# Optimization experiments

Hardware: AMD Instinct MI355X
Metric: run time of the kernel (lower is better)

Reference implementation:

```python
import jax, jax.numpy as jnp
import numpy as np

N, D, H, ED, E = 50000, 128, 4, 16, 800000
C = D // H  # 32 per-head channels


def setup_inputs() -> dict:
    key = jax.random.key(0)
    ks = jax.random.split(key, 12)
    w = lambda k, shape: jax.random.normal(k, shape, jnp.float32) * 0.05
    z = lambda: jnp.zeros((D,), jnp.float32)
    return dict(
        x=jax.random.normal(ks[0], (N, D), jnp.float32),
        edge_index=jax.random.randint(ks[1], (2, E), 0, N),
        edge_attr=jax.random.normal(ks[2], (E, ED), jnp.float32),
        Wq=w(ks[3], (D, D)), bq=z(),
        Wk=w(ks[4], (D, D)), bk=z(),
        Wv=w(ks[5], (D, D)), bv=z(),
        We=w(ks[6], (ED, D)),              # lin_edge, bias=False in PyG
        Ws=w(ks[7], (D, D)), bs=z(),       # TransformerConv root/skip lin
        Wsp=w(ks[8], (D, D)), bsp=z(),     # skip_proj
        Wg=w(ks[9], (2 * D, D)), bg=z(),   # gate linear
        g1=jnp.ones((D,), jnp.float32), b1=z(),
        g2=jnp.ones((D,), jnp.float32), b2=z(),
    )


def _ln(x, g, b):
    mu = x.mean(-1, keepdims=True)
    var = ((x - mu) ** 2).mean(-1, keepdims=True)
    return (x - mu) * jax.lax.rsqrt(var + 1e-5) * g + b


def reference(x, edge_index, edge_attr, Wq, bq, Wk, bk, Wv, bv, We, Ws, bs,
              Wsp, bsp, Wg, bg, g1, b1, g2, b2):
    src, dst = edge_index[0], edge_index[1]  # PyG: row=source j, col=target i
    q = (x @ Wq + bq).reshape(N, H, C)
    k = (x @ Wk + bk).reshape(N, H, C)
    v = (x @ Wv + bv).reshape(N, H, C)
    e = (edge_attr @ We).reshape(E, H, C)

    k_j = k[src] + e                                   # [E,H,C]
    alpha = (q[dst] * k_j).sum(-1) / np.sqrt(C)        # [E,H]
    # segment softmax over incoming edges of each target node
    m = jax.ops.segment_max(alpha, dst, num_segments=N)
    ea = jnp.exp(alpha - m[dst])
    denom = jax.ops.segment_sum(ea, dst, num_segments=N)
    a = ea / (denom[dst] + 1e-16)                      # [E,H]

    msg = (v[src] + e) * a[..., None]                  # [E,H,C]
    agg = jax.ops.segment_sum(msg, dst, num_segments=N).reshape(N, D)
    h = agg + x @ Ws + bs                              # root_weight skip

    h = jax.nn.gelu(_ln(h, g1, b1), approximate=False)  # norm1 + GELU (dropout=eval no-op)
    skip = x @ Wsp + bsp
    gate = jax.nn.sigmoid(jnp.concatenate([h, x], axis=1) @ Wg + bg)
    h = gate * h + (1.0 - gate) * skip
    return _ln(h, g2, b2)
```

## Files before the change

kernel.cpp:

```cpp
#include <hip/hip_runtime.h>
#include <hip/hip_bf16.h>

typedef short short8 __attribute__((ext_vector_type(8)));
typedef float f32x4 __attribute__((ext_vector_type(4)));

__device__ inline unsigned short f2bf(float x) {
  union { float f; unsigned u; } un; un.f = x;
  unsigned r = un.u + 0x7FFFu + ((un.u >> 16) & 1u);
  return (unsigned short)(r >> 16);
}
__device__ inline float bf2f(unsigned short u) {
  union { unsigned u; float f; } un; un.u = ((unsigned)u) << 16; return un.f;
}

__global__ void prep_weights(const float* __restrict__ Wq, const float* __restrict__ bq,
                             const float* __restrict__ Wk, const float* __restrict__ bk,
                             const float* __restrict__ Wv, const float* __restrict__ bv,
                             const float* __restrict__ Ws, const float* __restrict__ bs,
                             const float* __restrict__ Wsp, const float* __restrict__ bsp,
                             const float* __restrict__ Wg, const float* __restrict__ bg,
                             unsigned short* __restrict__ WcatT, unsigned short* __restrict__ WgTopT,
                             float* __restrict__ bcat) {
  int tid = blockIdx.x * 256 + threadIdx.x;
  if (tid >= 768 * 128) return;
  int n = tid >> 7, k = tid & 127;
  int s = n >> 7, c = n & 127;
  float val;
  if (s == 0) val = Wq[k * 128 + c];
  else if (s == 1) val = Wk[k * 128 + c];
  else if (s == 2) val = Wv[k * 128 + c];
  else if (s == 3) val = Ws[k * 128 + c];
  else if (s == 4) val = Wsp[k * 128 + c];
  else val = Wg[(128 + k) * 128 + c];
  WcatT[tid] = f2bf(val);
  if (n < 128) WgTopT[n * 128 + k] = f2bf(Wg[k * 128 + n]);
  if (k == 0) {
    float bv2;
    if (s == 0) bv2 = bq[c]; else if (s == 1) bv2 = bk[c]; else if (s == 2) bv2 = bv[c];
    else if (s == 3) bv2 = bs[c]; else if (s == 4) bv2 = bsp[c]; else bv2 = bg[c];
    bcat[n] = bv2;
  }
}

__global__ void prep_wefrag(const float* __restrict__ We, unsigned short* __restrict__ wf) {
  int id = blockIdx.x * 256 + threadIdx.x;
  if (id >= 4096) return;
  int j = id & 7, lane = (id >> 3) & 63, b = id >> 9;
  int t = (lane >> 4) * 8 + j;
  float v = (t < 16) ? We[t * 128 + b * 16 + (lane & 15)] : 0.0f;
  wf[id] = f2bf(v);
}

__global__ void convert_bf16(const float* __restrict__ x, unsigned short* __restrict__ xb, int n4) {
  int i = blockIdx.x * 256 + threadIdx.x;
  if (i < n4) {
    float4 v = ((const float4*)x)[i];
    ushort4 o;
    o.x = f2bf(v.x); o.y = f2bf(v.y); o.z = f2bf(v.z); o.w = f2bf(v.w);
    ((ushort4*)xb)[i] = o;
  }
}

__global__ void count_deg(const int* __restrict__ dst, int* __restrict__ deg, int E) {
  int i = blockIdx.x * 256 + threadIdx.x;
  if (i < E) atomicAdd(&deg[dst[i]], 1);
}

__global__ __launch_bounds__(256) void scan_bsum(const int* __restrict__ deg, int* __restrict__ bsum, int n) {
  __shared__ int red[256];
  int b = blockIdx.x, t = threadIdx.x;
  int base = b * 1024 + t * 4;
  int s = 0;
#pragma unroll
  for (int j = 0; j < 4; ++j) { int i = base + j; if (i < n) s += deg[i]; }
  red[t] = s; __syncthreads();
  for (int o = 128; o; o >>= 1) { if (t < o) red[t] += red[t + o]; __syncthreads(); }
  if (t == 0) bsum[b] = red[0];
}

__global__ void scan_top(int* __restrict__ bsum, int G) {
  int lane = threadIdx.x;
  int v = (lane < G) ? bsum[lane] : 0;
  int orig = v;
#pragma unroll
  for (int d = 1; d < 64; d <<= 1) { int u = __shfl_up(v, d); if (lane >= d) v += u; }
  if (lane < G) bsum[lane] = v - orig;
}

__global__ __launch_bounds__(256) void scan_write(const int* __restrict__ deg, const int* __restrict__ bsum,
                                                  int* __restrict__ off, int* __restrict__ cursor, int n) {
  __shared__ int red[256];
  int b = blockIdx.x, t = threadIdx.x;
  int base = b * 1024 + t * 4;
  int d0 = 0, d1 = 0, d2 = 0, d3 = 0;
  if (base + 3 < n) {
    int4 d4 = *(const int4*)(deg + base);
    d0 = d4.x; d1 = d4.y; d2 = d4.z; d3 = d4.w;
  } else {
    if (base + 0 < n) d0 = deg[base + 0];
    if (base + 1 < n) d1 = deg[base + 1];
    if (base + 2 < n) d2 = deg[base + 2];
    if (base + 3 < n) d3 = deg[base + 3];
  }
  int tsum = d0 + d1 + d2 + d3;
  red[t] = tsum; __syncthreads();
  for (int o = 1; o < 256; o <<= 1) {
    int val = (t >= o) ? red[t - o] : 0;
    __syncthreads();
    red[t] += val;
    __syncthreads();
  }
  int run = bsum[b] + red[t] - tsum;
  if (base + 0 < n) { off[base + 0] = run; cursor[base + 0] = run; run += d0; }
  if (base + 1 < n) { off[base + 1] = run; cursor[base + 1] = run; run += d1; }
  if (base + 2 < n) { off[base + 2] = run; cursor[base + 2] = run; run += d2; }
  if (base + 3 < n) { off[base + 3] = run; cursor[base + 3] = run; run += d3; }
  if (b == gridDim.x - 1 && t == 255) off[n] = run;
}

__global__ void scatter_kernel(const int* __restrict__ ei, int* __restrict__ cursor,
                               int2* __restrict__ slotsrc, int E) {
  int i = blockIdx.x * 256 + threadIdx.x;
  if (i < E) {
    int s = ei[i];
    int d = ei[E + i];
    int p = atomicAdd(&cursor[d], 1);
    slotsrc[p] = make_int2(i, s);
  }
}

__global__ __launch_bounds__(256) void gemm_fused(const unsigned short* __restrict__ A,
                                                  const unsigned short* __restrict__ BT,
                                                  const float* __restrict__ bias,
                                                  float* __restrict__ Y, int M) {
  __shared__ char As[32768];
  __shared__ char Bs[32768];
  int m0 = blockIdx.x * 128;
  int t = threadIdx.x;
  {
    int row = t >> 1;
    int hb = (t & 1) * 128;
    const char* srow = (const char*)(A + (size_t)(m0 + row) * 128);
    bool ok = (m0 + row) < M;
    char* lrow = As + row * 256;
    int sw = (row & 7) << 4;
#pragma unroll
    for (int j = 0; j < 8; ++j) {
      int b = hb + j * 16;
      uint4 val;
      if (ok) val = *(const uint4*)(srow + b);
      else { val.x = 0; val.y = 0; val.z = 0; val.w = 0; }
      *(uint4*)(lrow + (b ^ sw)) = val;
    }
  }
  int w = t >> 6, lane = t & 63;
  int lm = lane & 15, hi = lane >> 4;
  for (int nb = 0; nb < 6; ++nb) {
    __syncthreads();
    {
      int row = t >> 1;
      int hb = (t & 1) * 128;
      const char* srow = (const char*)(BT + (size_t)(nb * 128 + row) * 128);
      char* lrow = Bs + row * 256;
      int sw = (row & 7) << 4;
#pragma unroll
      for (int j = 0; j < 8; ++j) {
        int b = hb + j * 16;
        uint4 val = *(const uint4*)(srow + b);
        *(uint4*)(lrow + (b ^ sw)) = val;
      }
    }
    __syncthreads();
    f32x4 acc[2][8] = {};
#pragma unroll
    for (int kb = 0; kb < 4; ++kb) {
      int colb = kb * 64 + hi * 16;
      short8 a[2];
#pragma unroll
      for (int rf = 0; rf < 2; ++rf) {
        int row = w * 32 + rf * 16 + lm;
        a[rf] = *(const short8*)(As + row * 256 + (colb ^ ((row & 7) << 4)));
      }
#pragma unroll
      for (int cf = 0; cf < 8; ++cf) {
        int row = cf * 16 + lm;
        short8 bfr = *(const short8*)(Bs + row * 256 + (colb ^ ((row & 7) << 4)));
        acc[0][cf] = __builtin_amdgcn_mfma_f32_16x16x32_bf16(a[0], bfr, acc[0][cf], 0, 0, 0);
        acc[1][cf] = __builtin_amdgcn_mfma_f32_16x16x32_bf16(a[1], bfr, acc[1][cf], 0, 0, 0);
      }
    }
    bool to16 = (nb == 1 || nb == 2);
#pragma unroll
    for (int rf = 0; rf < 2; ++rf) {
#pragma unroll
      for (int cf = 0; cf < 8; ++cf) {
        int col = nb * 128 + cf * 16 + lm;
        float bv = bias[col];
#pragma unroll
        for (int j = 0; j < 4; ++j) {
          int row = m0 + w * 32 + rf * 16 + hi * 4 + j;
          if (row < M) {
            float val = acc[rf][cf][j] + bv;
            if (to16) {
              unsigned short* kvrow = (unsigned short*)((char*)Y + (size_t)row * 3072 + 512);
              kvrow[col - 128] = f2bf(val);
            } else {
              Y[(size_t)row * 768 + col] = val;
            }
          }
        }
      }
    }
  }
}

__global__ __launch_bounds__(256) void gemm_single(const unsigned short* __restrict__ A,
                                                   const unsigned short* __restrict__ BT,
                                                   float* __restrict__ C, int M) {
  __shared__ char As[32768];
  __shared__ char Bs[32768];
  int m0 = blockIdx.x * 128;
  int t = threadIdx.x;
  {
    int row = t >> 1;
    int hb = (t & 1) * 128;
    const char* srow = (const char*)(A + (size_t)(m0 + row) * 128);
    bool ok = (m0 + row) < M;
    char* lrow = As + row * 256;
    int sw = (row & 7) << 4;
#pragma unroll
    for (int j = 0; j < 8; ++j) {
      int b = hb + j * 16;
      uint4 val;
      if (ok) val = *(const uint4*)(srow + b);
      else { val.x = 0; val.y = 0; val.z = 0; val.w = 0; }
      *(uint4*)(lrow + (b ^ sw)) = val;
    }
  }
  {
    int row = t >> 1;
    int hb = (t & 1) * 128;
    const char* srow = (const char*)(BT + (size_t)row * 128);
    char* lrow = Bs + row * 256;
    int sw = (row & 7) << 4;
#pragma unroll
    for (int j = 0; j < 8; ++j) {
      int b = hb + j * 16;
      uint4 val = *(const uint4*)(srow + b);
      *(uint4*)(lrow + (b ^ sw)) = val;
    }
  }
  __syncthreads();
  int w = t >> 6, lane = t & 63;
  int lm = lane & 15, hi = lane >> 4;
  f32x4 acc[2][8] = {};
#pragma unroll
  for (int kb = 0; kb < 4; ++kb) {
    int colb = kb * 64 + hi * 16;
    short8 a[2];
#pragma unroll
    for (int rf = 0; rf < 2; ++rf) {
      int row = w * 32 + rf * 16 + lm;
      a[rf] = *(const short8*)(As + row * 256 + (colb ^ ((row & 7) << 4)));
    }
#pragma unroll
    for (int cf = 0; cf < 8; ++cf) {
      int row = cf * 16 + lm;
      short8 bfr = *(const short8*)(Bs + row * 256 + (colb ^ ((row & 7) << 4)));
      acc[0][cf] = __builtin_amdgcn_mfma_f32_16x16x32_bf16(a[0], bfr, acc[0][cf], 0, 0, 0);
      acc[1][cf] = __builtin_amdgcn_mfma_f32_16x16x32_bf16(a[1], bfr, acc[1][cf], 0, 0, 0);
    }
  }
#pragma unroll
  for (int rf = 0; rf < 2; ++rf) {
#pragma unroll
    for (int cf = 0; cf < 8; ++cf) {
      int col = cf * 16 + lm;
#pragma unroll
      for (int j = 0; j < 4; ++j) {
        int row = m0 + w * 32 + rf * 16 + hi * 4 + j;
        if (row < M) C[(size_t)row * 128 + col] = acc[rf][cf][j];
      }
    }
  }
}

__global__ __launch_bounds__(256) void edge_flash(const int2* __restrict__ slotsrc,
                                                  const int* __restrict__ off,
                                                  const unsigned short* __restrict__ attrb,
                                                  const unsigned short* __restrict__ wefrag,
                                                  const float* __restrict__ Y,
                                                  float* __restrict__ agg, int Nn) {
  int wv = threadIdx.x >> 6, lane = threadIdx.x & 63;
  int node = blockIdx.x * 4 + wv;
  if (node >= Nn) return;
  int esl = lane & 15, hi = lane >> 4;

  short8 weF[8];
#pragma unroll
  for (int b = 0; b < 8; ++b)
    weF[b] = *(const short8*)(wefrag + ((b * 64 + lane) << 3));

  float qv[8][4];
  const float* qrow = Y + (size_t)node * 768;
#pragma unroll
  for (int b = 0; b < 8; ++b) {
    float4 tq = *(const float4*)(qrow + 16 * b + 4 * hi);
    qv[b][0] = tq.x * 0.25505654f;
    qv[b][1] = tq.y * 0.25505654f;
    qv[b][2] = tq.z * 0.25505654f;
    qv[b][3] = tq.w * 0.25505654f;
  }

  float m[4], den[4], agr[8][4];
#pragma unroll
  for (int h = 0; h < 4; ++h) { m[h] = -INFINITY; den[h] = 0.0f; }
#pragma unroll
  for (int b = 0; b < 8; ++b)
#pragma unroll
    for (int r = 0; r < 4; ++r) agr[b][r] = 0.0f;

  int beg = off[node], end = off[node + 1];
  for (int p0 = beg; p0 < end; p0 += 16) {
    int pidx = p0 + esl;
    bool valid = pidx < end;
    if (!valid) pidx = end - 1;
    int2 ss = slotsrc[pidx];

    short8 fb = (short8){0, 0, 0, 0, 0, 0, 0, 0};
    if (hi < 2) fb = *(const short8*)(attrb + ((size_t)ss.x << 4) + (hi << 3));

    f32x4 accE[8];
#pragma unroll
    for (int b = 0; b < 8; ++b) {
      f32x4 z = {0.0f, 0.0f, 0.0f, 0.0f};
      accE[b] = __builtin_amdgcn_mfma_f32_16x16x32_bf16(weF[b], fb, z, 0, 0, 0);
    }

    const char* kvb = (const char*)Y + (size_t)ss.y * 3072 + 512 + (hi << 3);
    float ph[4] = {0.0f, 0.0f, 0.0f, 0.0f};
#pragma unroll
    for (int b = 0; b < 8; ++b) {
      ushort4 kk = *(const ushort4*)(kvb + (b << 5));
      int h = b >> 1;
      ph[h] = fmaf(qv[b][0], bf2f(kk.x) + accE[b][0], ph[h]);
      ph[h] = fmaf(qv[b][1], bf2f(kk.y) + accE[b][1], ph[h]);
      ph[h] = fmaf(qv[b][2], bf2f(kk.z) + accE[b][2], ph[h]);
      ph[h] = fmaf(qv[b][3], bf2f(kk.w) + accE[b][3], ph[h]);
    }
#pragma unroll
    for (int h = 0; h < 4; ++h) {
      ph[h] += __shfl_xor(ph[h], 16);
      ph[h] += __shfl_xor(ph[h], 32);
      if (!valid) ph[h] = -3.0e38f;
    }
    float p[4], sc[4];
#pragma unroll
    for (int h = 0; h < 4; ++h) {
      float tm = ph[h];
      tm = fmaxf(tm, __shfl_xor(tm, 1));
      tm = fmaxf(tm, __shfl_xor(tm, 2));
      tm = fmaxf(tm, __shfl_xor(tm, 4));
      tm = fmaxf(tm, __shfl_xor(tm, 8));
      float mn = fmaxf(m[h], tm);
      sc[h] = exp2f(m[h] - mn);
      p[h] = exp2f(ph[h] - mn);
      m[h] = mn;
      den[h] = den[h] * sc[h] + p[h];
    }
#pragma unroll
    for (int b = 0; b < 8; ++b) {
      ushort4 vv = *(const ushort4*)(kvb + 256 + (b << 5));
      int h = b >> 1;
      float pr = p[h], s = sc[h];
      agr[b][0] = agr[b][0] * s + pr * (bf2f(vv.x) + accE[b][0]);
      agr[b][1] = agr[b][1] * s + pr * (bf2f(vv.y) + accE[b][1]);
      agr[b][2] = agr[b][2] * s + pr * (bf2f(vv.z) + accE[b][2]);
      agr[b][3] = agr[b][3] * s + pr * (bf2f(vv.w) + accE[b][3]);
    }
  }

#pragma unroll
  for (int h = 0; h < 4; ++h) {
    den[h] += __shfl_xor(den[h], 1);
    den[h] += __shfl_xor(den[h], 2);
    den[h] += __shfl_xor(den[h], 4);
    den[h] += __shfl_xor(den[h], 8);
  }
#pragma unroll
  for (int b = 0; b < 8; ++b)
#pragma unroll
    for (int r = 0; r < 4; ++r) {
      agr[b][r] += __shfl_xor(agr[b][r], 1);
      agr[b][r] += __shfl_xor(agr[b][r], 2);
      agr[b][r] += __shfl_xor(agr[b][r], 4);
      agr[b][r] += __shfl_xor(agr[b][r], 8);
    }
  float rden[4];
#pragma unroll
  for (int h = 0; h < 4; ++h) rden[h] = 1.0f / (den[h] + 1e-16f);

  int id0 = esl * 2;
  float v0 = 0.0f, v1 = 0.0f;
#pragma unroll
  for (int b = 0; b < 8; ++b)
#pragma unroll
    for (int r = 0; r < 4; ++r) {
      int id = b * 4 + r;
      float tv = agr[b][r] * rden[b >> 1];
      if (id == id0) v0 = tv;
      if (id == id0 + 1) v1 = tv;
    }
  int c0 = (id0 >> 2) * 16 + hi * 4 + (id0 & 3);
  float* arow = agg + (size_t)node * 128;
  arow[c0] = v0;
  arow[c0 + 1] = v1;
}

__global__ __launch_bounds__(256) void ln_gelu_kernel(const float* __restrict__ agg,
                                                      const float* __restrict__ Y,
                                                      const float* __restrict__ g1,
                                                      const float* __restrict__ b1,
                                                      float* __restrict__ u,
                                                      unsigned short* __restrict__ ub, int Nn) {
  int w = threadIdx.x >> 6, lane = threadIdx.x & 63;
  int row = blockIdx.x * 4 + w;
  if (row >= Nn) return;
  const float* yrow = Y + (size_t)row * 768 + 384;
  const float* arow = agg + (size_t)row * 128;
  float h0 = arow[lane] + yrow[lane];
  float h1 = arow[lane + 64] + yrow[lane + 64];
  float s = h0 + h1;
#pragma unroll
  for (int o = 32; o; o >>= 1) s += __shfl_xor(s, o, 64);
  float mean = s * (1.0f / 128.0f);
  float d0 = h0 - mean, d1 = h1 - mean;
  float ss = d0 * d0 + d1 * d1;
#pragma unroll
  for (int o = 32; o; o >>= 1) ss += __shfl_xor(ss, o, 64);
  float rs = rsqrtf(ss * (1.0f / 128.0f) + 1e-5f);
  float y0 = d0 * rs * g1[lane] + b1[lane];
  float y1 = d1 * rs * g1[lane + 64] + b1[lane + 64];
  float u0 = 0.5f * y0 * (1.0f + erff(y0 * 0.7071067811865475f));
  float u1 = 0.5f * y1 * (1.0f + erff(y1 * 0.7071067811865475f));
  size_t base = (size_t)row * 128;
  u[base + lane] = u0;
  u[base + lane + 64] = u1;
  ub[base + lane] = f2bf(u0);
  ub[base + lane + 64] = f2bf(u1);
}

__global__ __launch_bounds__(256) void gate_ln_kernel(const float* __restrict__ gate_u,
                                                      const float* __restrict__ Y,
                                                      const float* __restrict__ u,
                                                      const float* __restrict__ g2,
                                                      const float* __restrict__ b2,
                                                      float* __restrict__ out, int Nn) {
  int w = threadIdx.x >> 6, lane = threadIdx.x & 63;
  int row = blockIdx.x * 4 + w;
  if (row >= Nn) return;
  const float* yrow = Y + (size_t)row * 768;
  size_t base = (size_t)row * 128;
  float z0 = gate_u[base + lane] + yrow[640 + lane];
  float z1 = gate_u[base + lane + 64] + yrow[640 + lane + 64];
  float gg0 = 1.0f / (1.0f + __expf(-z0));
  float gg1 = 1.0f / (1.0f + __expf(-z1));
  float u0 = u[base + lane], u1 = u[base + lane + 64];
  float s0 = yrow[512 + lane], s1 = yrow[512 + lane + 64];
  float h0 = gg0 * u0 + (1.0f - gg0) * s0;
  float h1 = gg1 * u1 + (1.0f - gg1) * s1;
  float s = h0 + h1;
#pragma unroll
  for (int o = 32; o; o >>= 1) s += __shfl_xor(s, o, 64);
  float mean = s * (1.0f / 128.0f);
  float d0 = h0 - mean, d1 = h1 - mean;
  float ss = d0 * d0 + d1 * d1;
#pragma unroll
  for (int o = 32; o; o >>= 1) ss += __shfl_xor(ss, o, 64);
  float rs = rsqrtf(ss * (1.0f / 128.0f) + 1e-5f);
  out[base + lane] = d0 * rs * g2[lane] + b2[lane];
  out[base + lane + 64] = d1 * rs * g2[lane + 64] + b2[lane + 64];
}

extern "C" void kernel_launch(void* const* d_in, const int* in_sizes, int n_in,
                              void* d_out, int out_size, void* d_ws, size_t ws_size,
                              hipStream_t stream) {
  const float* x = (const float*)d_in[0];
  const int* edge_index = (const int*)d_in[1];
  const float* edge_attr = (const float*)d_in[2];
  const float* Wq = (const float*)d_in[3];
  const float* bq = (const float*)d_in[4];
  const float* Wk = (const float*)d_in[5];
  const float* bk = (const float*)d_in[6];
  const float* Wv = (const float*)d_in[7];
  const float* bv = (const float*)d_in[8];
  const float* We = (const float*)d_in[9];
  const float* Ws = (const float*)d_in[10];
  const float* bs = (const float*)d_in[11];
  const float* Wsp = (const float*)d_in[12];
  const float* bsp = (const float*)d_in[13];
  const float* Wg = (const float*)d_in[14];
  const float* bg = (const float*)d_in[15];
  const float* g1 = (const float*)d_in[16];
  const float* b1 = (const float*)d_in[17];
  const float* g2 = (const float*)d_in[18];
  const float* b2 = (const float*)d_in[19];

  int Nn = in_sizes[0] / 128;
  int E = in_sizes[1] / 2;

  char* p = (char*)d_ws;
  auto align256 = [](size_t b) { return (b + 255) & ~(size_t)255; };
  auto alloc = [&](size_t bytes) -> char* {
    char* r = p;
    p += align256(bytes);
    return r;
  };
  float* Y = (float*)alloc((size_t)Nn * 768 * 4);
  float* agg = (float*)alloc((size_t)Nn * 128 * 4);
  unsigned short* WcatT = (unsigned short*)alloc(768 * 128 * 2);
  unsigned short* WgTopT = (unsigned short*)alloc(128 * 128 * 2);
  unsigned short* wefrag = (unsigned short*)alloc(4096 * 2);
  float* bcat = (float*)alloc(768 * 4);
  int* off = (int*)alloc((size_t)(Nn + 1) * 4);

  size_t earlySz = align256((size_t)Nn * 128 * 2)
                 + align256((size_t)E * 16 * 2)
                 + align256((size_t)E * 8)
                 + align256((size_t)Nn * 4)
                 + align256((size_t)Nn * 4)
                 + align256(256 * 4);
  size_t lateSz = align256((size_t)Nn * 128 * 4)
                + align256((size_t)Nn * 128 * 2)
                + align256((size_t)Nn * 128 * 4);
  char* arena = alloc(earlySz > lateSz ? earlySz : lateSz);

  char* q = arena;
  auto ealloc = [&](size_t bytes) -> char* { char* r = q; q += align256(bytes); return r; };
  unsigned short* xb = (unsigned short*)ealloc((size_t)Nn * 128 * 2);
  unsigned short* attrb = (unsigned short*)ealloc((size_t)E * 16 * 2);
  int2* slotsrc = (int2*)ealloc((size_t)E * 8);
  int* deg = (int*)ealloc((size_t)Nn * 4);
  int* cursor = (int*)ealloc((size_t)Nn * 4);
  int* bsum = (int*)ealloc(256 * 4);

  q = arena;
  float* u = (float*)ealloc((size_t)Nn * 128 * 4);
  unsigned short* ub = (unsigned short*)ealloc((size_t)Nn * 128 * 2);
  float* gate_u = (float*)ealloc((size_t)Nn * 128 * 4);

  hipMemsetAsync(deg, 0, (size_t)Nn * 4, stream);
  prep_weights<<<(768 * 128 + 255) / 256, 256, 0, stream>>>(Wq, bq, Wk, bk, Wv, bv, Ws, bs,
                                                            Wsp, bsp, Wg, bg, WcatT, WgTopT, bcat);
  prep_wefrag<<<16, 256, 0, stream>>>(We, wefrag);
  convert_bf16<<<((Nn * 128 / 4) + 255) / 256, 256, 0, stream>>>(x, xb, Nn * 128 / 4);
  convert_bf16<<<((E * 16 / 4) + 255) / 256, 256, 0, stream>>>(edge_attr, attrb, E * 16 / 4);
  count_deg<<<(E + 255) / 256, 256, 0, stream>>>(edge_index + E, deg, E);

  int G = (Nn + 1023) >> 10;
  scan_bsum<<<G, 256, 0, stream>>>(deg, bsum, Nn);
  scan_top<<<1, 64, 0, stream>>>(bsum, G);
  scan_write<<<G, 256, 0, stream>>>(deg, bsum, off, cursor, Nn);
  scatter_kernel<<<(E + 255) / 256, 256, 0, stream>>>(edge_index, cursor, slotsrc, E);

  gemm_fused<<<(Nn + 127) / 128, 256, 0, stream>>>(xb, WcatT, bcat, Y, Nn);

  edge_flash<<<(Nn + 3) / 4, 256, 0, stream>>>(slotsrc, off, attrb, wefrag, Y, agg, Nn);

  ln_gelu_kernel<<<(Nn + 3) / 4, 256, 0, stream>>>(agg, Y, g1, b1, u, ub, Nn);

  gemm_single<<<(Nn + 127) / 128, 256, 0, stream>>>(ub, WgTopT, gate_u, Nn);

  gate_ln_kernel<<<(Nn + 3) / 4, 256, 0, stream>>>(gate_u, Y, u, g2, b2, (float*)d_out, Nn);
}
```

Before: 458.0 us.

## Split edge attention across two waves per node by head pair, prefetch indices

Each target node is now handled by two wavefronts, one per pair of heads, instead of one wavefront covering all four heads. This halves per-wave registers and serial work per edge, which should raise occupancy and parallelism on this latency-bound gather kernel. The next edge-slot indices are also prefetched one iteration ahead, and K/V loads are issued before the MFMA to overlap memory latency. The cost is duplicated edge_attr loads and MFMA work per edge across the two waves, plus twice as many waves launched.

```diff
diff --git a/kernel.cpp b/kernel.cpp
--- a/kernel.cpp
+++ b/kernel.cpp
@@ -292,71 +292,84 @@
                                                   const float* __restrict__ Y,
                                                   float* __restrict__ agg, int Nn) {
   int wv = threadIdx.x >> 6, lane = threadIdx.x & 63;
-  int node = blockIdx.x * 4 + wv;
+  int node = blockIdx.x * 2 + (wv >> 1);
   if (node >= Nn) return;
+  int hf = wv & 1;
   int esl = lane & 15, hi = lane >> 4;
 
-  short8 weF[8];
-#pragma unroll
-  for (int b = 0; b < 8; ++b)
-    weF[b] = *(const short8*)(wefrag + ((b * 64 + lane) << 3));
-
-  float qv[8][4];
-  const float* qrow = Y + (size_t)node * 768;
-#pragma unroll
-  for (int b = 0; b < 8; ++b) {
-    float4 tq = *(const float4*)(qrow + 16 * b + 4 * hi);
-    qv[b][0] = tq.x * 0.25505654f;
-    qv[b][1] = tq.y * 0.25505654f;
-    qv[b][2] = tq.z * 0.25505654f;
-    qv[b][3] = tq.w * 0.25505654f;
-  }
-
-  float m[4], den[4], agr[8][4];
-#pragma unroll
-  for (int h = 0; h < 4; ++h) { m[h] = -INFINITY; den[h] = 0.0f; }
-#pragma unroll
-  for (int b = 0; b < 8; ++b)
-#pragma unroll
-    for (int r = 0; r < 4; ++r) agr[b][r] = 0.0f;
+  short8 weF[4];
+#pragma unroll
+  for (int bp = 0; bp < 4; ++bp)
+    weF[bp] = *(const short8*)(wefrag + (((hf * 4 + bp) * 64 + lane) << 3));
+
+  float qv[4][4];
+  const float* qrow = Y + (size_t)node * 768 + hf * 64;
+#pragma unroll
+  for (int bp = 0; bp < 4; ++bp) {
+    float4 tq = *(const float4*)(qrow + 16 * bp + 4 * hi);
+    qv[bp][0] = tq.x * 0.25505654f;
+    qv[bp][1] = tq.y * 0.25505654f;
+    qv[bp][2] = tq.z * 0.25505654f;
+    qv[bp][3] = tq.w * 0.25505654f;
+  }
+
+  float m[2], den[2], agr[4][4];
+#pragma unroll
+  for (int h = 0; h < 2; ++h) { m[h] = -INFINITY; den[h] = 0.0f; }
+#pragma unroll
+  for (int bp = 0; bp < 4; ++bp)
+#pragma unroll
+    for (int r = 0; r < 4; ++r) agr[bp][r] = 0.0f;
 
   int beg = off[node], end = off[node + 1];
+
+  int2 ssA;
+  if (beg < end) {
+    int idx = beg + esl; if (idx >= end) idx = end - 1;
+    ssA = slotsrc[idx];
+  }
   for (int p0 = beg; p0 < end; p0 += 16) {
-    int pidx = p0 + esl;
-    bool valid = pidx < end;
-    if (!valid) pidx = end - 1;
-    int2 ss = slotsrc[pidx];
-
+    int2 ss = ssA;
+    bool valid = (p0 + esl) < end;
+    if (p0 + 16 < end) {
+      int idx = p0 + 16 + esl; if (idx >= end) idx = end - 1;
+      ssA = slotsrc[idx];
+    }
+    const char* kvb = (const char*)Y + (size_t)ss.y * 3072 + 512 + hf * 128 + (hi << 3);
+    ushort4 kk[4], vv[4];
+#pragma unroll
+    for (int bp = 0; bp < 4; ++bp) {
+      kk[bp] = *(const ushort4*)(kvb + (bp << 5));
+      vv[bp] = *(const ushort4*)(kvb + 256 + (bp << 5));
+    }
     short8 fb = (short8){0, 0, 0, 0, 0, 0, 0, 0};
     if (hi < 2) fb = *(const short8*)(attrb + ((size_t)ss.x << 4) + (hi << 3));
 
-    f32x4 accE[8];
-#pragma unroll
-    for (int b = 0; b < 8; ++b) {
+    f32x4 accE[4];
+#pragma unroll
+    for (int bp = 0; bp < 4; ++bp) {
       f32x4 z = {0.0f, 0.0f, 0.0f, 0.0f};
-      accE[b] = __builtin_amdgcn_mfma_f32_16x16x32_bf16(weF[b], fb, z, 0, 0, 0);
-    }
-
-    const char* kvb = (const char*)Y + (size_t)ss.y * 3072 + 512 + (hi << 3);
-    float ph[4] = {0.0f, 0.0f, 0.0f, 0.0f};
-#pragma unroll
-    for (int b = 0; b < 8; ++b) {
-      ushort4 kk = *(const ushort4*)(kvb + (b << 5));
-      int h = b >> 1;
-      ph[h] = fmaf(qv[b][0], bf2f(kk.x) + accE[b][0], ph[h]);
-      ph[h] = fmaf(qv[b][1], bf2f(kk.y) + accE[b][1], ph[h]);
-      ph[h] = fmaf(qv[b][2], bf2f(kk.z) + accE[b][2], ph[h]);
-      ph[h] = fmaf(qv[b][3], bf2f(kk.w) + accE[b][3], ph[h]);
-    }
-#pragma unroll
-    for (int h = 0; h < 4; ++h) {
+      accE[bp] = __builtin_amdgcn_mfma_f32_16x16x32_bf16(weF[bp], fb, z, 0, 0, 0);
+    }
+
+    float ph[2] = {0.0f, 0.0f};
+#pragma unroll
+    for (int bp = 0; bp < 4; ++bp) {
+      int h = bp >> 1;
+      ph[h] = fmaf(qv[bp][0], bf2f(kk[bp].x) + accE[bp][0], ph[h]);
+      ph[h] = fmaf(qv[bp][1], bf2f(kk[bp].y) + accE[bp][1], ph[h]);
+      ph[h] = fmaf(qv[bp][2], bf2f(kk[bp].z) + accE[bp][2], ph[h]);
+      ph[h] = fmaf(qv[bp][3], bf2f(kk[bp].w) + accE[bp][3], ph[h]);
+    }
+#pragma unroll
+    for (int h = 0; h < 2; ++h) {
       ph[h] += __shfl_xor(ph[h], 16);
       ph[h] += __shfl_xor(ph[h], 32);
       if (!valid) ph[h] = -3.0e38f;
     }
-    float p[4], sc[4];
-#pragma unroll
-    for (int h = 0; h < 4; ++h) {
+    float p[2], sc[2];
+#pragma unroll
+    for (int h = 0; h < 2; ++h) {
       float tm = ph[h];
       tm = fmaxf(tm, __shfl_xor(tm, 1));
       tm = fmaxf(tm, __shfl_xor(tm, 2));
@@ -369,52 +382,47 @@
       den[h] = den[h] * sc[h] + p[h];
     }
 #pragma unroll
-    for (int b = 0; b < 8; ++b) {
-      ushort4 vv = *(const ushort4*)(kvb + 256 + (b << 5));
-      int h = b >> 1;
+    for (int bp = 0; bp < 4; ++bp) {
+      int h = bp >> 1;
       float pr = p[h], s = sc[h];
-      agr[b][0] = agr[b][0] * s + pr * (bf2f(vv.x) + accE[b][0]);
-      agr[b][1] = agr[b][1] * s + pr * (bf2f(vv.y) + accE[b][1]);
-      agr[b][2] = agr[b][2] * s + pr * (bf2f(vv.z) + accE[b][2]);
-      agr[b][3] = agr[b][3] * s + pr * (bf2f(vv.w) + accE[b][3]);
-    }
-  }
-
-#pragma unroll
-  for (int h = 0; h < 4; ++h) {
+      agr[bp][0] = agr[bp][0] * s + pr * (bf2f(vv[bp].x) + accE[bp][0]);
+      agr[bp][1] = agr[bp][1] * s + pr * (bf2f(vv[bp].y) + accE[bp][1]);
+      agr[bp][2] = agr[bp][2] * s + pr * (bf2f(vv[bp].z) + accE[bp][2]);
+      agr[bp][3] = agr[bp][3] * s + pr * (bf2f(vv[bp].w) + accE[bp][3]);
+    }
+  }
+
+#pragma unroll
+  for (int h = 0; h < 2; ++h) {
     den[h] += __shfl_xor(den[h], 1);
     den[h] += __shfl_xor(den[h], 2);
     den[h] += __shfl_xor(den[h], 4);
     den[h] += __shfl_xor(den[h], 8);
   }
 #pragma unroll
-  for (int b = 0; b < 8; ++b)
+  for (int bp = 0; bp < 4; ++bp)
 #pragma unroll
     for (int r = 0; r < 4; ++r) {
-      agr[b][r] += __shfl_xor(agr[b][r], 1);
-      agr[b][r] += __shfl_xor(agr[b][r], 2);
-      agr[b][r] += __shfl_xor(agr[b][r], 4);
-      agr[b][r] += __shfl_xor(agr[b][r], 8);
-    }
-  float rden[4];
-#pragma unroll
-  for (int h = 0; h < 4; ++h) rden[h] = 1.0f / (den[h] + 1e-16f);
-
-  int id0 = esl * 2;
-  float v0 = 0.0f, v1 = 0.0f;
-#pragma unroll
-  for (int b = 0; b < 8; ++b)
+      agr[bp][r] += __shfl_xor(agr[bp][r], 1);
+      agr[bp][r] += __shfl_xor(agr[bp][r], 2);
+      agr[bp][r] += __shfl_xor(agr[bp][r], 4);
+      agr[bp][r] += __shfl_xor(agr[bp][r], 8);
+    }
+  float rden[2];
+#pragma unroll
+  for (int h = 0; h < 2; ++h) rden[h] = 1.0f / (den[h] + 1e-16f);
+
+  float v0 = 0.0f;
+#pragma unroll
+  for (int bp = 0; bp < 4; ++bp)
 #pragma unroll
     for (int r = 0; r < 4; ++r) {
-      int id = b * 4 + r;
-      float tv = agr[b][r] * rden[b >> 1];
-      if (id == id0) v0 = tv;
-      if (id == id0 + 1) v1 = tv;
-    }
-  int c0 = (id0 >> 2) * 16 + hi * 4 + (id0 & 3);
-  float* arow = agg + (size_t)node * 128;
-  arow[c0] = v0;
-  arow[c0 + 1] = v1;
+      int id = bp * 4 + r;
+      float tv = agr[bp][r] * rden[bp >> 1];
+      if (id == esl) v0 = tv;
+    }
+  int c = hf * 64 + (esl >> 2) * 16 + hi * 4 + (esl & 3);
+  agg[(size_t)node * 128 + c] = v0;
 }
 
 __global__ __launch_bounds__(256) void ln_gelu_kernel(const float* __restrict__ agg,
@@ -565,7 +573,7 @@
 
   gemm_fused<<<(Nn + 127) / 128, 256, 0, stream>>>(xb, WcatT, bcat, Y, Nn);
 
-  edge_flash<<<(Nn + 3) / 4, 256, 0, stream>>>(slotsrc, off, attrb, wefrag, Y, agg, Nn);
+  edge_flash<<<(Nn + 1) / 2, 256, 0, stream>>>(slotsrc, off, attrb, wefrag, Y, agg, Nn);
 
   ln_gelu_kernel<<<(Nn + 3) / 4, 256, 0, stream>>>(agg, Y, g1, b1, u, ub, Nn);
 
```

Result: faster. 402.4 us (-12.1%).
